# Performance work log

Hardware: AMD Instinct MI355X
Metric: run time of the kernel (lower is better)

Reference implementation:

```python
import jax, jax.numpy as jnp
import numpy as np

ALPHA = 0.2          # LeakyReLU negative slope
NEG_INF = -9e15      # mask value used by the original module


def setup_inputs() -> dict:
    key = jax.random.key(0)
    k1, k2, k3, k4 = jax.random.split(key, 4)
    N, F_IN, F_OUT = 8192, 512, 256
    inp = jax.random.normal(k1, (N, F_IN), dtype=jnp.float32)
    W = jax.random.normal(k2, (F_IN, F_OUT), dtype=jnp.float32) * (1.414 / np.sqrt(F_IN))
    a = jax.random.normal(k3, (2 * F_OUT, 1), dtype=jnp.float32) * (1.414 / np.sqrt(F_OUT))
    adj = jax.random.randint(k4, (N, N), 0, 2, dtype=jnp.int32)
    return {"input": inp, "W": W, "a": a, "adj": adj}


def reference(input, W, a, adj):
    # h: [N, F_out]
    h = input @ W
    F_out = h.shape[1]
    # Original builds a_input[i,j] = concat(h_i, h_j) then matmuls with a.
    # Equivalent: e_ij = leakyrelu(h_i . a[:F] + h_j . a[F:]) without the O(N^2 * 2F) tensor.
    a1 = a[:F_out, 0]   # [F_out]
    a2 = a[F_out:, 0]   # [F_out]
    s1 = h @ a1         # [N]
    s2 = h @ a2         # [N]
    e = jax.nn.leaky_relu(s1[:, None] + s2[None, :], negative_slope=ALPHA)  # [N, N]
    attention = jax.nn.softmax(jnp.where(adj > 0, e, NEG_INF), axis=1)       # [N, N]
    return attention @ h  # [N, F_out]
```

## Files before the change

kernel.cpp:

```cpp
#include <hip/hip_runtime.h>


typedef __attribute__((ext_vector_type(8))) short bf16x8;
typedef __attribute__((ext_vector_type(4))) float fx4;
typedef __attribute__((ext_vector_type(4))) int ix4;
typedef __attribute__((ext_vector_type(2))) unsigned int ux2;

#define NN 8192
#define FIN 512
#define FOUT 256
#define PS 136
#define AROWS 64

__device__ __forceinline__ unsigned short f2bf(float f) {
    unsigned int x = __float_as_uint(f);
    x += 0x7fffu + ((x >> 16) & 1u);
    return (unsigned short)(x >> 16);
}
__device__ __forceinline__ bf16x8 pack8(fx4 a, fx4 b) {
    bf16x8 r;
    r[0] = (short)f2bf(a[0]); r[1] = (short)f2bf(a[1]);
    r[2] = (short)f2bf(a[2]); r[3] = (short)f2bf(a[3]);
    r[4] = (short)f2bf(b[0]); r[5] = (short)f2bf(b[1]);
    r[6] = (short)f2bf(b[2]); r[7] = (short)f2bf(b[3]);
    return r;
}

__global__ void wt_kernel(const float* __restrict__ W,
                          unsigned short* __restrict__ WTt) {
    const int c = threadIdx.x;
    const int k = blockIdx.x;
    WTt[((size_t)(k >> 5) * 256 + c) * 32 + (k & 31)] = f2bf(W[k * FOUT + c]);
}

__global__ __launch_bounds__(256) void prep_kernel(
    const float* __restrict__ X,
    const unsigned short* __restrict__ WTt,
    const float* __restrict__ A,
    unsigned short* __restrict__ hTt,
    float* __restrict__ s1, float* __restrict__ s2)
{
    __shared__ float s1sh[4][16], s2sh[4][16];
    const int tid = threadIdx.x;

    const int w = tid >> 6, l = tid & 63, q = l >> 4, lr = l & 15;
    const int r0 = blockIdx.x * 16;
    const int cbase = w * 64;
    fx4 acc[4] = {};

    for (int kb = 0; kb < FIN; kb += 32) {
        const float* xp = X + (size_t)(r0 + lr) * FIN + kb + q * 8;
        bf16x8 a0 = pack8(*(const fx4*)xp, *(const fx4*)(xp + 4));
#pragma unroll
        for (int tc = 0; tc < 4; ++tc) {
            bf16x8 b = *(const bf16x8*)(WTt + ((size_t)(kb >> 5) * 256 + cbase + tc * 16 + lr) * 32 + q * 8);
            acc[tc] = __builtin_amdgcn_mfma_f32_16x16x32_bf16(a0, b, acc[tc], 0, 0, 0);
        }
    }

    const int jb = r0 >> 5, jo = (r0 & 31) + q * 4;
#pragma unroll
    for (int tc = 0; tc < 4; ++tc) {
        const int c = cbase + tc * 16 + lr;
        ux2 hp;
        hp.x = (unsigned)f2bf(acc[tc][0]) | ((unsigned)f2bf(acc[tc][1]) << 16);
        hp.y = (unsigned)f2bf(acc[tc][2]) | ((unsigned)f2bf(acc[tc][3]) << 16);
        *(ux2*)(hTt + ((size_t)jb * 256 + c) * 32 + jo) = hp;
    }

    float p1[4] = {}, p2[4] = {};
#pragma unroll
    for (int tc = 0; tc < 4; ++tc) {
        const int c = cbase + tc * 16 + lr;
        const float a1v = A[c], a2v = A[FOUT + c];
#pragma unroll
        for (int r = 0; r < 4; ++r) {
            p1[r] += acc[tc][r] * a1v;
            p2[r] += acc[tc][r] * a2v;
        }
    }
#pragma unroll
    for (int r = 0; r < 4; ++r) {
#pragma unroll
        for (int off = 1; off < 16; off <<= 1) {
            p1[r] += __shfl_xor(p1[r], off);
            p2[r] += __shfl_xor(p2[r], off);
        }
        if (lr == 0) { s1sh[w][q * 4 + r] = p1[r]; s2sh[w][q * 4 + r] = p2[r]; }
    }
    __syncthreads();
    if (tid < 16) {
        s1[r0 + tid] = s1sh[0][tid] + s1sh[1][tid] + s1sh[2][tid] + s1sh[3][tid];
        s2[r0 + tid] = s2sh[0][tid] + s2sh[1][tid] + s2sh[2][tid] + s2sh[3][tid];
    }
}

__global__ __launch_bounds__(512) void attn_kernel(
    const int* __restrict__ adj,
    const unsigned short* __restrict__ hTt,
    const float* __restrict__ s1,
    const float* __restrict__ s2,
    float* __restrict__ out)
{
    __shared__ unsigned short P[2][AROWS * PS];
    __shared__ float dsh[AROWS];

    const int tid = threadIdx.x;
    const int rg = blockIdx.x >> 1;
    const int ch = blockIdx.x & 1;
    const int r0 = rg * AROWS;
    const int c0 = ch * 128;

    const int prow = tid >> 3;
    const int pq = tid & 7;
    const float s1v = s1[r0 + prow];
    const int* arow = adj + (size_t)(r0 + prow) * NN + pq * 8;
    float denp = 0.f;

    const int w = tid >> 6, l = tid & 63, q = l >> 4, lr = l & 15;
    const int rgw = (w >> 2) * 32;
    const int cbase = c0 + (w & 3) * 32;
    fx4 acc[2][2] = {};

    struct LSet { ix4 v0, v1; fx4 s2a, s2b; };
    LSet SA, SB;
    bf16x8 B0[4][2], B1[4][2];

    auto loadS = [&](int kt, int kq, LSet& L) {
        const int* ap = arow + kt * 128 + kq * 64;
        L.v0 = __builtin_nontemporal_load((const ix4*)ap);
        L.v1 = __builtin_nontemporal_load((const ix4*)(ap + 4));
        L.s2a = *(const fx4*)(s2 + kt * 128 + kq * 64 + pq * 8);
        L.s2b = *(const fx4*)(s2 + kt * 128 + kq * 64 + pq * 8 + 4);
    };
    auto calcP = [&](int b, int kq, const LSet& L) {
        bf16x8 pv;
#pragma unroll
        for (int j = 0; j < 8; ++j) {
            const int aj = (j < 4) ? L.v0[j] : L.v1[j - 4];
            const float s2j = (j < 4) ? L.s2a[j] : L.s2b[j - 4];
            float t = s1v + s2j;
            float e = fmaxf(t, 0.2f * t);
            e = fminf(e, 30.f);
            const float p = (aj != 0) ? __expf(e) : 0.f;
            denp += p;
            pv[j] = (short)f2bf(p);
        }
        *(bf16x8*)(&P[b][prow * PS + kq * 64 + pq * 8]) = pv;
    };
    auto loadB = [&](int it, bf16x8 (&B)[4][2]) {
#pragma unroll
        for (int ks = 0; ks < 4; ++ks)
#pragma unroll
            for (int tc = 0; tc < 2; ++tc)
                B[ks][tc] = *(const bf16x8*)(hTt + ((size_t)(it * 4 + ks) * 256 + cbase + tc * 16 + lr) * 32 + q * 8);
    };

    auto ldsBarrier = [&]() {
        asm volatile("s_waitcnt lgkmcnt(0)" ::: "memory");
        __builtin_amdgcn_s_barrier();
    };

    const int ITERS = NN / 128;
    loadS(0, 0, SA); loadS(0, 1, SB);
    calcP(0, 0, SA); calcP(0, 1, SB);
    loadS(1, 0, SA); loadS(1, 1, SB);
    loadB(0, B0);
    ldsBarrier();

    auto body = [&](int it, bf16x8 (&Bc)[4][2], bf16x8 (&Bn)[4][2]) {
        if (it + 1 < ITERS) loadB(it + 1, Bn);
        const unsigned short* Pb = P[it & 1];
        bf16x8 af0[4], af1[4];
#pragma unroll
        for (int ks = 0; ks < 4; ++ks) {
            af0[ks] = *(const bf16x8*)(Pb + (rgw + lr) * PS + ks * 32 + q * 8);
            af1[ks] = *(const bf16x8*)(Pb + (rgw + 16 + lr) * PS + ks * 32 + q * 8);
        }
        __builtin_amdgcn_s_setprio(1);
#pragma unroll
        for (int ks = 0; ks < 4; ++ks)
#pragma unroll
            for (int tc = 0; tc < 2; ++tc) {
                acc[0][tc] = __builtin_amdgcn_mfma_f32_16x16x32_bf16(af0[ks], Bc[ks][tc], acc[0][tc], 0, 0, 0);
                acc[1][tc] = __builtin_amdgcn_mfma_f32_16x16x32_bf16(af1[ks], Bc[ks][tc], acc[1][tc], 0, 0, 0);
            }
        __builtin_amdgcn_s_setprio(0);
        if (it + 1 < ITERS) {
            calcP((it + 1) & 1, 0, SA);
            calcP((it + 1) & 1, 1, SB);
        }
        if (it + 2 < ITERS) {
            loadS(it + 2, 0, SA);
            loadS(it + 2, 1, SB);
        }
        ldsBarrier();
    };

    for (int it = 0; it < ITERS; it += 2) {
        body(it, B0, B1);
        body(it + 1, B1, B0);
    }

    float v = denp;
    v += __shfl_xor(v, 1);
    v += __shfl_xor(v, 2);
    v += __shfl_xor(v, 4);
    if (pq == 0) dsh[prow] = v;
    __syncthreads();

#pragma unroll
    for (int mg = 0; mg < 2; ++mg) {
#pragma unroll
        for (int r = 0; r < 4; ++r) {
            const int row = rgw + mg * 16 + q * 4 + r;
            const float dinv = 1.0f / fmaxf(dsh[row], 1e-30f);
#pragma unroll
            for (int tc = 0; tc < 2; ++tc) {
                out[(size_t)(r0 + row) * FOUT + cbase + tc * 16 + lr] = acc[mg][tc][r] * dinv;
            }
        }
    }
}

extern "C" void kernel_launch(void* const* d_in, const int* in_sizes, int n_in,
                              void* d_out, int out_size, void* d_ws, size_t ws_size,
                              hipStream_t stream) {
    const float *X = nullptr, *W = nullptr, *A = nullptr;
    const int* adj = nullptr;
    for (int i = 0; i < n_in; ++i) {
        switch (in_sizes[i]) {
            case NN * FIN:   X = (const float*)d_in[i]; break;
            case FIN * FOUT: W = (const float*)d_in[i]; break;
            case 2 * FOUT:   A = (const float*)d_in[i]; break;
            case NN * NN:    adj = (const int*)d_in[i]; break;
        }
    }
    if (!X) X = (const float*)d_in[0];
    if (!W) W = (const float*)d_in[1];
    if (!A) A = (const float*)d_in[2];
    if (!adj) adj = (const int*)d_in[3];
    float* out = (float*)d_out;

    char* ws = (char*)d_ws;
    float* s1 = (float*)ws;
    float* s2 = (float*)(ws + 32768);
    unsigned short* WTt = (unsigned short*)(ws + 98304);
    unsigned short* hTt = (unsigned short*)(ws + 360448);

    wt_kernel<<<512, 256, 0, stream>>>(W, WTt);
    prep_kernel<<<512, 256, 0, stream>>>(X, WTt, A, hTt, s1, s2);
    attn_kernel<<<(NN / AROWS) * 2, 512, 0, stream>>>(adj, hTt, s1, s2, out);
}
```

Measured before the change: 475.1 us.

## Split attention over K halves instead of output columns, add combine kernel

New measurement: 413.3 us. 13.0% less time.

```diff
diff --git a/kernel.cpp b/kernel.cpp
--- a/kernel.cpp
+++ b/kernel.cpp
@@ -95,43 +95,42 @@
     }
 }
 
-__global__ __launch_bounds__(512) void attn_kernel(
+__global__ __launch_bounds__(512, 2) void attn_kernel(
     const int* __restrict__ adj,
     const unsigned short* __restrict__ hTt,
     const float* __restrict__ s1,
     const float* __restrict__ s2,
-    float* __restrict__ out)
+    float* __restrict__ num,
+    float* __restrict__ den)
 {
     __shared__ unsigned short P[2][AROWS * PS];
-    __shared__ float dsh[AROWS];
-
     const int tid = threadIdx.x;
     const int rg = blockIdx.x >> 1;
-    const int ch = blockIdx.x & 1;
+    const int kh = blockIdx.x & 1;
     const int r0 = rg * AROWS;
-    const int c0 = ch * 128;
+    const int khB = kh * 32;
 
     const int prow = tid >> 3;
     const int pq = tid & 7;
     const float s1v = s1[r0 + prow];
-    const int* arow = adj + (size_t)(r0 + prow) * NN + pq * 8;
+    const int* arow = adj + (size_t)(r0 + prow) * NN + (size_t)kh * 4096 + pq * 8;
     float denp = 0.f;
 
     const int w = tid >> 6, l = tid & 63, q = l >> 4, lr = l & 15;
-    const int rgw = (w >> 2) * 32;
-    const int cbase = c0 + (w & 3) * 32;
-    fx4 acc[2][2] = {};
+    const int cbase = w * 32;
+    fx4 acc[4][2] = {};
 
     struct LSet { ix4 v0, v1; fx4 s2a, s2b; };
     LSet SA, SB;
     bf16x8 B0[4][2], B1[4][2];
 
-    auto loadS = [&](int kt, int kq, LSet& L) {
-        const int* ap = arow + kt * 128 + kq * 64;
+    auto loadS = [&](int s, int kq, LSet& L) {
+        const int* ap = arow + s * 128 + kq * 64;
         L.v0 = __builtin_nontemporal_load((const ix4*)ap);
         L.v1 = __builtin_nontemporal_load((const ix4*)(ap + 4));
-        L.s2a = *(const fx4*)(s2 + kt * 128 + kq * 64 + pq * 8);
-        L.s2b = *(const fx4*)(s2 + kt * 128 + kq * 64 + pq * 8 + 4);
+        const float* sp = s2 + (khB + s) * 128 + kq * 64 + pq * 8;
+        L.s2a = *(const fx4*)sp;
+        L.s2b = *(const fx4*)(sp + 4);
     };
     auto calcP = [&](int b, int kq, const LSet& L) {
         bf16x8 pv;
@@ -148,12 +147,13 @@
         }
         *(bf16x8*)(&P[b][prow * PS + kq * 64 + pq * 8]) = pv;
     };
-    auto loadB = [&](int it, bf16x8 (&B)[4][2]) {
+    auto loadB = [&](int s, bf16x8 (&B)[4][2]) {
+        const int kt = khB + s;
 #pragma unroll
         for (int ks = 0; ks < 4; ++ks)
 #pragma unroll
             for (int tc = 0; tc < 2; ++tc)
-                B[ks][tc] = *(const bf16x8*)(hTt + ((size_t)(it * 4 + ks) * 256 + cbase + tc * 16 + lr) * 32 + q * 8);
+                B[ks][tc] = *(const bf16x8*)(hTt + ((size_t)(kt * 4 + ks) * 256 + cbase + tc * 16 + lr) * 32 + q * 8);
     };
 
     auto ldsBarrier = [&]() {
@@ -161,7 +161,8 @@
         __builtin_amdgcn_s_barrier();
     };
 
-    const int ITERS = NN / 128;
+    const int ITERS = 32;
+
     loadS(0, 0, SA); loadS(0, 1, SB);
     calcP(0, 0, SA); calcP(0, 1, SB);
     loadS(1, 0, SA); loadS(1, 1, SB);
@@ -171,21 +172,20 @@
     auto body = [&](int it, bf16x8 (&Bc)[4][2], bf16x8 (&Bn)[4][2]) {
         if (it + 1 < ITERS) loadB(it + 1, Bn);
         const unsigned short* Pb = P[it & 1];
-        bf16x8 af0[4], af1[4];
-#pragma unroll
-        for (int ks = 0; ks < 4; ++ks) {
-            af0[ks] = *(const bf16x8*)(Pb + (rgw + lr) * PS + ks * 32 + q * 8);
-            af1[ks] = *(const bf16x8*)(Pb + (rgw + 16 + lr) * PS + ks * 32 + q * 8);
-        }
-        __builtin_amdgcn_s_setprio(1);
-#pragma unroll
-        for (int ks = 0; ks < 4; ++ks)
-#pragma unroll
-            for (int tc = 0; tc < 2; ++tc) {
-                acc[0][tc] = __builtin_amdgcn_mfma_f32_16x16x32_bf16(af0[ks], Bc[ks][tc], acc[0][tc], 0, 0, 0);
-                acc[1][tc] = __builtin_amdgcn_mfma_f32_16x16x32_bf16(af1[ks], Bc[ks][tc], acc[1][tc], 0, 0, 0);
-            }
-        __builtin_amdgcn_s_setprio(0);
+#pragma unroll
+        for (int rg4 = 0; rg4 < 4; ++rg4) {
+            bf16x8 af[4];
+#pragma unroll
+            for (int ks = 0; ks < 4; ++ks)
+                af[ks] = *(const bf16x8*)(Pb + (rg4 * 16 + lr) * PS + ks * 32 + q * 8);
+            __builtin_amdgcn_s_setprio(1);
+#pragma unroll
+            for (int ks = 0; ks < 4; ++ks)
+#pragma unroll
+                for (int tc = 0; tc < 2; ++tc)
+                    acc[rg4][tc] = __builtin_amdgcn_mfma_f32_16x16x32_bf16(af[ks], Bc[ks][tc], acc[rg4][tc], 0, 0, 0);
+            __builtin_amdgcn_s_setprio(0);
+        }
         if (it + 1 < ITERS) {
             calcP((it + 1) & 1, 0, SA);
             calcP((it + 1) & 1, 1, SB);
@@ -206,21 +206,33 @@
     v += __shfl_xor(v, 1);
     v += __shfl_xor(v, 2);
     v += __shfl_xor(v, 4);
-    if (pq == 0) dsh[prow] = v;
-    __syncthreads();
-
-#pragma unroll
-    for (int mg = 0; mg < 2; ++mg) {
+    if (pq == 0) den[(size_t)kh * NN + r0 + prow] = v;
+
+    float* nb = num + (size_t)kh * NN * FOUT;
+#pragma unroll
+    for (int rg4 = 0; rg4 < 4; ++rg4)
 #pragma unroll
         for (int r = 0; r < 4; ++r) {
-            const int row = rgw + mg * 16 + q * 4 + r;
-            const float dinv = 1.0f / fmaxf(dsh[row], 1e-30f);
-#pragma unroll
-            for (int tc = 0; tc < 2; ++tc) {
-                out[(size_t)(r0 + row) * FOUT + cbase + tc * 16 + lr] = acc[mg][tc][r] * dinv;
-            }
-        }
-    }
+            const int row = rg4 * 16 + q * 4 + r;
+#pragma unroll
+            for (int tc = 0; tc < 2; ++tc)
+                nb[(size_t)(r0 + row) * FOUT + cbase + tc * 16 + lr] = acc[rg4][tc][r];
+        }
+}
+
+__global__ __launch_bounds__(512) void combine_kernel(
+    const float* __restrict__ num, const float* __restrict__ den,
+    float* __restrict__ out)
+{
+    const int idx = blockIdx.x * 512 + threadIdx.x;
+    const int r = idx >> 6;
+    const fx4 a = *(const fx4*)(num + (size_t)idx * 4);
+    const fx4 b = *(const fx4*)(num + (size_t)NN * FOUT + (size_t)idx * 4);
+    const float dinv = 1.0f / fmaxf(den[r] + den[NN + r], 1e-30f);
+    fx4 o;
+#pragma unroll
+    for (int j = 0; j < 4; ++j) o[j] = (a[j] + b[j]) * dinv;
+    *(fx4*)(out + (size_t)idx * 4) = o;
 }
 
 extern "C" void kernel_launch(void* const* d_in, const int* in_sizes, int n_in,
@@ -247,8 +259,11 @@
     float* s2 = (float*)(ws + 32768);
     unsigned short* WTt = (unsigned short*)(ws + 98304);
     unsigned short* hTt = (unsigned short*)(ws + 360448);
+    float* num = (float*)(ws + 8388608);
+    float* den = (float*)(ws + 25165824);
 
     wt_kernel<<<512, 256, 0, stream>>>(W, WTt);
     prep_kernel<<<512, 256, 0, stream>>>(X, WTt, A, hTt, s1, s2);
-    attn_kernel<<<(NN / AROWS) * 2, 512, 0, stream>>>(adj, hTt, s1, s2, out);
-}
+    attn_kernel<<<(NN / AROWS) * 2, 512, 0, stream>>>(adj, hTt, s1, s2, num, den);
+    combine_kernel<<<1024, 512, 0, stream>>>(num, den, out);
+}
```
